# Kernel tuning notes

Measured on AMD Instinct MI355X. Metric: run time of the kernel, lower is better.

Reference implementation:

```python
import jax, jax.numpy as jnp
import numpy as np

B, S, HID, NH = 64, 197, 768, 12
DH = HID // NH  # 64
EPS = 1e-24


def setup_inputs() -> dict:
    key = jax.random.key(0)
    ks = jax.random.split(key, 20)
    def lin(i):
        w = jax.random.normal(ks[i], (HID, HID), jnp.float32) * 0.02  # stored [in, out]
        b = jnp.zeros((HID,), jnp.float32)
        return w, b
    Wmq, bmq = lin(0); Wcq, bcq = lin(1)
    Wmk, bmk = lin(2); Wck, bck = lin(3)
    Wmv, bmv = lin(4); Wcv, bcv = lin(5)
    Wmd, bmd = lin(6); Wcd, bcd = lin(7)
    return dict(
        input_mean_tensor=jax.random.normal(ks[8], (B, S, HID), jnp.float32),
        input_cov_tensor=jax.random.normal(ks[9], (B, S, HID), jnp.float32),
        Wmq=Wmq, bmq=bmq, Wcq=Wcq, bcq=bcq,
        Wmk=Wmk, bmk=bmk, Wck=Wck, bck=bck,
        Wmv=Wmv, bmv=bmv, Wcv=Wcv, bcv=bcv,
        Wmd=Wmd, bmd=bmd, Wcd=Wcd, bcd=bcd,
    )


def _heads(x):
    # [B, S, HID] -> [B, NH, S, DH]
    return x.reshape(x.shape[0], x.shape[1], NH, DH).transpose(0, 2, 1, 3)


def _merge(x):
    # [B, NH, S, DH] -> [B, S, HID]
    return x.transpose(0, 2, 1, 3).reshape(x.shape[0], x.shape[2], HID)


def wasserstein_distance_matmul(m1, c1, m2, c2):
    # all [B, NH, S, DH]; returns [B, NH, S, S]
    m1_2 = jnp.sum(m1 * m1, -1, keepdims=True)            # [B,NH,S,1]
    m2_2 = jnp.sum(m2 * m2, -1, keepdims=True)
    ret = m1_2 + jnp.swapaxes(m2_2, -1, -2) - 2.0 * jnp.einsum('bhqd,bhkd->bhqk', m1, m2)
    c1_2 = jnp.sum(c1, -1, keepdims=True)
    c2_2 = jnp.sum(c2, -1, keepdims=True)
    s1 = jnp.sqrt(jnp.clip(c1, EPS, None))
    s2 = jnp.sqrt(jnp.clip(c2, EPS, None))
    cov_ret = c1_2 + jnp.swapaxes(c2_2, -1, -2) - 2.0 * jnp.einsum('bhqd,bhkd->bhqk', s1, s2)
    return ret + cov_ret


def reference(input_mean_tensor, input_cov_tensor,
              Wmq, bmq, Wcq, bcq, Wmk, bmk, Wck, bck,
              Wmv, bmv, Wcv, bcv, Wmd, bmd, Wcd, bcd):
    mean_q = _heads(input_mean_tensor @ Wmq + bmq)
    mean_k = _heads(input_mean_tensor @ Wmk + bmk)
    mean_v = _heads(input_mean_tensor @ Wmv + bmv)
    cov_q = _heads(jax.nn.elu(input_cov_tensor @ Wcq + bcq) + 1.0)
    cov_k = _heads(jax.nn.elu(input_cov_tensor @ Wck + bck) + 1.0)
    cov_v = _heads(jax.nn.elu(input_cov_tensor @ Wcv + bcv) + 1.0)

    scores = -wasserstein_distance_matmul(mean_q, cov_q, mean_k, cov_k)
    scores = scores / jnp.sqrt(jnp.float32(DH))
    probs = jax.nn.softmax(scores, axis=-1)  # [B,NH,S,S]

    mean_ctx = _merge(jnp.einsum('bhqk,bhkd->bhqd', probs, mean_v))
    cov_ctx = _merge(jnp.einsum('bhqk,bhkd->bhqd', probs * probs, cov_v))

    mean_hidden = mean_ctx @ Wmd + bmd
    cov_hidden = cov_ctx @ Wcd + bcd
    return (mean_hidden, cov_hidden)
```

## Files before the change

### kernel.cpp

```cpp
#include <hip/hip_runtime.h>
#include <hip/hip_bf16.h>
#include <stdint.h>

typedef _Float16 f16;
typedef _Float16 f16x8 __attribute__((ext_vector_type(8)));
typedef _Float16 f16x4 __attribute__((ext_vector_type(4)));
typedef float f32x4 __attribute__((ext_vector_type(4)));

constexpr int B = 64, S = 197, HID = 768, NH = 12, DH = 64;
constexpr int M = B * S;
constexpr int Mpad = 12800;
constexpr int BNS = B * NH * S;
constexpr int VSTRIDE = 224;
constexpr size_t NPH = (size_t)Mpad * HID;
constexpr size_t MH = (size_t)M * HID;
constexpr size_t WSZ1 = (size_t)HID * HID;
constexpr size_t VTSZ = (size_t)B * NH * DH * VSTRIDE;

__device__ __forceinline__ f32x4 mfma16(f16x8 a, f16x8 b, f32x4 c) {
  return __builtin_amdgcn_mfma_f32_16x16x32_f16(a, b, c, 0, 0, 0);
}

__device__ __forceinline__ void gload16(const void* g, void* l) {
  __builtin_amdgcn_global_load_lds(
      (const __attribute__((address_space(1))) void*)g,
      (__attribute__((address_space(3))) void*)l, 16, 0, 0);
}

__device__ __forceinline__ int xcd_swizzle(int wg, int nwg) {
  const int q = nwg >> 3, r = nwg & 7;
  const int x = wg & 7, p = wg >> 3;
  return (x < r ? x * (q + 1) : r * (q + 1) + (x - r) * q) + p;
}

__global__ __launch_bounds__(256) void zero_kernel(char* __restrict__ p, size_t n16) {
  const size_t i = (size_t)blockIdx.x * 256 + threadIdx.x;
  if (i < n16) reinterpret_cast<int4*>(p)[i] = int4{0, 0, 0, 0};
}

__global__ __launch_bounds__(256) void cvt_x_kernel(
    const float* __restrict__ xm, const float* __restrict__ xc,
    f16* __restrict__ ym, f16* __restrict__ yc) {
  const size_t i8 = ((size_t)blockIdx.x * 256 + threadIdx.x) * 8;
  f16x8 vm = {}, vc = {};
  if (i8 < MH) {
    const float4 a0 = *reinterpret_cast<const float4*>(xm + i8);
    const float4 a1 = *reinterpret_cast<const float4*>(xm + i8 + 4);
    const float4 b0 = *reinterpret_cast<const float4*>(xc + i8);
    const float4 b1 = *reinterpret_cast<const float4*>(xc + i8 + 4);
    vm[0] = (f16)a0.x; vm[1] = (f16)a0.y; vm[2] = (f16)a0.z; vm[3] = (f16)a0.w;
    vm[4] = (f16)a1.x; vm[5] = (f16)a1.y; vm[6] = (f16)a1.z; vm[7] = (f16)a1.w;
    vc[0] = (f16)b0.x; vc[1] = (f16)b0.y; vc[2] = (f16)b0.z; vc[3] = (f16)b0.w;
    vc[4] = (f16)b1.x; vc[5] = (f16)b1.y; vc[6] = (f16)b1.z; vc[7] = (f16)b1.w;
  }
  *reinterpret_cast<f16x8*>(ym + i8) = vm;
  *reinterpret_cast<f16x8*>(yc + i8) = vc;
}

struct WPtrs { const float* w[8]; };

__global__ __launch_bounds__(256) void cvt_w_kernel(WPtrs p, f16* __restrict__ wt) {
  __shared__ float tile[32][33];
  const int z = blockIdx.z;
  const float* W = p.w[z];
  f16* Wt = wt + (size_t)z * WSZ1;
  const int k0 = blockIdx.x * 32, n0 = blockIdx.y * 32;
  const int tx = threadIdx.x & 31, ty = threadIdx.x >> 5;
#pragma unroll
  for (int i = 0; i < 4; ++i)
    tile[ty + i * 8][tx] = W[(size_t)(k0 + ty + i * 8) * HID + n0 + tx];
  __syncthreads();
#pragma unroll
  for (int i = 0; i < 4; ++i)
    Wt[(size_t)(n0 + ty + i * 8) * HID + k0 + tx] = (f16)tile[tx][ty + i * 8];
}

__device__ __forceinline__ void gemm_core(
    const f16* __restrict__ Abase, const f16* __restrict__ Btbase,
    int m0, int n0, int tid, char* lds, f32x4 (&acc)[4][4]) {
  const int w = tid >> 6, lane = tid & 63;
  const int l15 = lane & 15, lg = lane >> 4;
  const int wr = (w >> 2) * 64, wc = (w & 3) * 64;

  const int arow = w * 16 + (lane >> 2);
  const int brow = w * 32 + (lane >> 2);
  const int scol = (((lane & 3) ^ ((lane >> 3) & 3)) * 16);
  const char* gA = reinterpret_cast<const char*>(Abase + (size_t)(m0 + arow) * HID) + scol;
  const char* gB = reinterpret_cast<const char*>(Btbase + (size_t)(n0 + brow) * HID) + scol;

  const int rslot = ((lg ^ (l15 >> 1)) & 3) * 16;

#define STAGE_TILE(T, BUF)                                               \
  do {                                                                   \
    const size_t off_ = (size_t)(T) * 64;                                \
    char* bp_ = lds + (BUF) * 24576;                                     \
    gload16(gA + off_, bp_ + w * 1024);                                  \
    gload16(gB + off_, bp_ + 8192 + w * 2048);                           \
    gload16(gB + off_ + (size_t)16 * 1536, bp_ + 8192 + w * 2048 + 1024);\
  } while (0)

  STAGE_TILE(0, 0);
  STAGE_TILE(1, 1);
  asm volatile("s_waitcnt vmcnt(3)\n\ts_barrier" ::: "memory");

#pragma unroll
  for (int t = 0; t < 24; ++t) {
    if (t + 2 < 24) STAGE_TILE(t + 2, (t + 2) % 3);

    const char* cb = lds + (t % 3) * 24576;
    f16x8 af[4], bf[4];
#pragma unroll
    for (int fi = 0; fi < 4; ++fi)
      af[fi] = *reinterpret_cast<const f16x8*>(cb + (wr + l15 + fi * 16) * 64 + rslot);
#pragma unroll
    for (int fj = 0; fj < 4; ++fj)
      bf[fj] = *reinterpret_cast<const f16x8*>(
          cb + 8192 + (wc + l15 + fj * 16) * 64 + rslot);

    __builtin_amdgcn_s_setprio(1);
#pragma unroll
    for (int fi = 0; fi < 4; ++fi)
#pragma unroll
      for (int fj = 0; fj < 4; ++fj)
        acc[fi][fj] = mfma16(af[fi], bf[fj], acc[fi][fj]);
    __builtin_amdgcn_s_setprio(0);

    if (t + 2 < 24) {
      asm volatile("s_waitcnt vmcnt(3)\n\ts_barrier" ::: "memory");
    } else if (t + 1 < 24) {
      asm volatile("s_waitcnt vmcnt(0)\n\ts_barrier" ::: "memory");
    }
  }
#undef STAGE_TILE
}

struct ProjArgs {
  const f16* A[2]; const f16* Bt[2];
  const float* bias[2][3];
  f16* out0[2];
  f16* out1[2];
  f16* vt[2];
  float* qterm; float* kterm;
};

template <int Z>
__global__ __launch_bounds__(512, 2) void gemm_proj(ProjArgs g) {
  __shared__ alignas(16) char lds[73728];
  const int swz = xcd_swizzle(blockIdx.x, 900);
  const int x = swz / 9, y = swz - x * 9;
  const int m0 = x * 128, n0 = y * 256;

  f32x4 acc[4][4] = {};
  gemm_core(g.A[Z], g.Bt[Z], m0, n0, threadIdx.x, lds, acc);

  const int tid = threadIdx.x, w = tid >> 6, lane = tid & 63;
  const int l15 = lane & 15, lg = lane >> 4;
  const int wr = (w >> 2) * 64, wc = (w & 3) * 64;
  const int nsel = n0 / 768;
  const int colbase = (n0 - nsel * 768) + wc;
  const int rbase = m0 + wr + lg * 4;
  const float* bias = g.bias[Z][nsel];

  if (nsel < 2) {
    const int hh = colbase >> 6;
    f16* Y = nsel ? g.out1[Z] : g.out0[Z];
    float* term = nsel ? g.kterm : g.qterm;
    float bv4[4];
#pragma unroll
    for (int fj = 0; fj < 4; ++fj) bv4[fj] = bias[colbase + l15 + fj * 16];
#pragma unroll
    for (int fi = 0; fi < 4; ++fi) {
#pragma unroll
      for (int r = 0; r < 4; ++r) {
        const int row = rbase + fi * 16 + r;
        float ssum = 0.f;
#pragma unroll
        for (int fj = 0; fj < 4; ++fj) {
          float v = acc[fi][fj][r] + bv4[fj];
          if (Z == 1) { v = (v > 0.f) ? v + 1.f : __expf(v); v = sqrtf(v); }
          const f16 st = (f16)(v * 0.5f);
          if (row < M) Y[(size_t)row * HID + colbase + l15 + fj * 16] = st;
          const float sf = (float)st;
          ssum = fmaf(sf, sf, ssum);
        }
        ssum += __shfl_xor(ssum, 1, 64);
        ssum += __shfl_xor(ssum, 2, 64);
        ssum += __shfl_xor(ssum, 4, 64);
        ssum += __shfl_xor(ssum, 8, 64);
        if (l15 == 0 && row < M) {
          const int bb = row / S, ss = row - bb * S;
          atomicAdd(&term[(bb * NH + hh) * S + ss], 0.5f * ssum);
        }
      }
    }
  } else {
    f16* VT = g.vt[Z];
    f16* LT = reinterpret_cast<f16*>(lds);
    __syncthreads();
#pragma unroll
    for (int fj = 0; fj < 4; ++fj) {
      const int c = wc + l15 + fj * 16;
      const float bv = bias[colbase - wc + c];
#pragma unroll
      for (int fi = 0; fi < 4; ++fi)
#pragma unroll
        for (int r = 0; r < 4; ++r) {
          const int rl = wr - (wr & 64) + 0;
          (void)rl;
          float v = acc[fi][fj][r] + bv;
          if (Z == 1) v = (v > 0.f) ? v + 1.f : __expf(v);
          const int row_local = wr + lg * 4 + fi * 16 + r;
          LT[(size_t)c * 136 + row_local] = (f16)v;
        }
    }
    __syncthreads();
    const int rh = w >> 2;
    const int cw = w & 3;
    const int row_local = rh * 64 + lane;
    const int grow = m0 + row_local;
    if (grow < M) {
      const int bb = grow / S;
      const int ss = grow - bb * S;
      const int vb = n0 - 1536;
#pragma unroll 8
      for (int k = 0; k < 64; ++k) {
        const int c = cw * 64 + k;
        const int vcol = vb + c;
        const int hh = vcol >> 6, dd = vcol & 63;
        const f16 v = LT[(size_t)c * 136 + row_local];
        VT[((size_t)(bb * NH + hh) * DH + dd) * VSTRIDE + ss] = v;
      }
    }
  }
}

struct OutArgs {
  const f16* A[2]; const f16* Bt[2]; const float* bias[2]; float* Y[2];
};

template <int Z>
__global__ __launch_bounds__(512, 2) void gemm_out(OutArgs g) {
  __shared__ alignas(16) char lds[73728];
  const int swz = xcd_swizzle(blockIdx.x, 300);
  const int x = swz / 3, y = swz - x * 3;
  const int m0 = x * 128, n0 = y * 256;

  f32x4 acc[4][4] = {};
  gemm_core(g.A[Z], g.Bt[Z], m0, n0, threadIdx.x, lds, acc);

  const int tid = threadIdx.x, w = tid >> 6, lane = tid & 63;
  const int l15 = lane & 15, lg = lane >> 4;
  const int wr = (w >> 2) * 64, wc = (w & 3) * 64;
  const int rbase = m0 + wr + lg * 4;
  float* Y = g.Y[Z];
#pragma unroll
  for (int fj = 0; fj < 4; ++fj) {
    const int col = n0 + wc + l15 + fj * 16;
    const float bv = g.bias[Z][col];
#pragma unroll
    for (int fi = 0; fi < 4; ++fi)
#pragma unroll
      for (int r = 0; r < 4; ++r) {
        const int row = rbase + fi * 16 + r;
        if (row < M) Y[(size_t)row * HID + col] = acc[fi][fj][r] + bv;
      }
  }
}

__global__ __launch_bounds__(256, 2) void attn_kernel(
    const f16* __restrict__ mq, const f16* __restrict__ sq,
    const f16* __restrict__ mk, const f16* __restrict__ sk,
    const f16* __restrict__ vtm, const f16* __restrict__ vtc,
    const float* __restrict__ qterm, const float* __restrict__ kterm,
    f16* __restrict__ mean_ctx, f16* __restrict__ cov_ctx) {
  __shared__ char Pb[64 * 512];
  __shared__ float qt_s[64];
  __shared__ float kt_s[256];
  __shared__ float red_m[4][64];
  __shared__ float red_s[4][64];

  const int swz = xcd_swizzle(blockIdx.x, 3072);
  const int qtile = swz & 3, bh = swz >> 2;
  const int h = bh % NH, b = bh / NH;
  const int s0 = qtile * 64;
  const int tid = threadIdx.x, w = tid >> 6, lane = tid & 63;
  const int l15 = lane & 15, lg = lane >> 4;

  const size_t base = (size_t)(b * S) * HID + (size_t)h * DH;
  const int tb = bh * S;

  f16x8 qmf[4][2], qsf[4][2];
#pragma unroll
  for (int fi = 0; fi < 4; ++fi) {
    const size_t o = base + (size_t)(s0 + fi * 16 + l15) * HID + lg * 8;
    qmf[fi][0] = *reinterpret_cast<const f16x8*>(mq + o);
    qmf[fi][1] = *reinterpret_cast<const f16x8*>(mq + o + 32);
    qsf[fi][0] = *reinterpret_cast<const f16x8*>(sq + o);
    qsf[fi][1] = *reinterpret_cast<const f16x8*>(sq + o + 32);
  }
  if (tid < 64) qt_s[tid] = (s0 + tid < S) ? qterm[tb + s0 + tid] : 0.f;
  kt_s[tid] = (tid < S) ? kterm[tb + tid] : 0.f;
  __syncthreads();

  f32x4 acc[4][4] = {};
  __builtin_amdgcn_s_setprio(1);
#pragma unroll
  for (int fj = 0; fj < 4; ++fj) {
    const size_t o = base + (size_t)(w * 64 + fj * 16 + l15) * HID + lg * 8;
    const f16x8 a0 = *reinterpret_cast<const f16x8*>(mk + o);
    const f16x8 a1 = *reinterpret_cast<const f16x8*>(mk + o + 32);
    const f16x8 c0 = *reinterpret_cast<const f16x8*>(sk + o);
    const f16x8 c1 = *reinterpret_cast<const f16x8*>(sk + o + 32);
#pragma unroll
    for (int fi = 0; fi < 4; ++fi) {
      acc[fj][fi] = mfma16(a0, qmf[fi][0], acc[fj][fi]);
      acc[fj][fi] = mfma16(c0, qsf[fi][0], acc[fj][fi]);
      acc[fj][fi] = mfma16(a1, qmf[fi][1], acc[fj][fi]);
      acc[fj][fi] = mfma16(c1, qsf[fi][1], acc[fj][fi]);
    }
  }
  __builtin_amdgcn_s_setprio(0);

  const int d = w * 16 + l15;
  const size_t vbase = ((size_t)bh * DH + d) * VSTRIDE + lg * 8;
  f16x8 vmr[7], vcr[7];
#pragma unroll
  for (int ks = 0; ks < 7; ++ks) {
    vmr[ks] = *reinterpret_cast<const f16x8*>(vtm + vbase + ks * 32);
    vcr[ks] = *reinterpret_cast<const f16x8*>(vtc + vbase + ks * 32);
  }

#pragma unroll
  for (int fi = 0; fi < 4; ++fi) {
    const float qv = qt_s[fi * 16 + l15];
    float mx = -1e30f;
#pragma unroll
    for (int fj = 0; fj < 4; ++fj)
#pragma unroll
      for (int r = 0; r < 4; ++r) {
        const int j = w * 64 + fj * 16 + lg * 4 + r;
        float sv = acc[fj][fi][r] - qv - kt_s[j];
        if (j >= S) sv = -1e30f;
        acc[fj][fi][r] = sv;
        mx = fmaxf(mx, sv);
      }
    mx = fmaxf(mx, __shfl_xor(mx, 16, 64));
    mx = fmaxf(mx, __shfl_xor(mx, 32, 64));
    if (lg == 0) red_m[w][fi * 16 + l15] = mx;
  }
  __syncthreads();

#pragma unroll
  for (int fi = 0; fi < 4; ++fi) {
    const int q = fi * 16 + l15;
    const float m = fmaxf(fmaxf(red_m[0][q], red_m[1][q]),
                          fmaxf(red_m[2][q], red_m[3][q]));
    const int xr = (q & 7) << 4;
    float sum = 0.f;
#pragma unroll
    for (int fj = 0; fj < 4; ++fj) {
      f16x4 p4;
#pragma unroll
      for (int r = 0; r < 4; ++r) {
        const float e = __expf(acc[fj][fi][r] - m);
        sum += e;
        p4[r] = (f16)e;
      }
      *reinterpret_cast<f16x4*>(
          Pb + q * 512 + ((2 * (w * 64 + fj * 16 + lg * 4)) ^ xr)) = p4;
    }
    sum += __shfl_xor(sum, 16, 64);
    sum += __shfl_xor(sum, 32, 64);
    if (lg == 0) red_s[w][q] = sum;
  }
  __syncthreads();

  f32x4 macc[4] = {}, cacc[4] = {};
  __builtin_amdgcn_s_setprio(1);
#pragma unroll
  for (int ks = 0; ks < 7; ++ks) {
#pragma unroll
    for (int fi = 0; fi < 4; ++fi) {
      const int q = fi * 16 + l15;
      const f16x8 pa = *reinterpret_cast<const f16x8*>(
          Pb + q * 512 + ((2 * (ks * 32 + lg * 8)) ^ ((q & 7) << 4)));
      macc[fi] = mfma16(pa, vmr[ks], macc[fi]);
      const f16x8 pq = pa * pa;
      cacc[fi] = mfma16(pq, vcr[ks], cacc[fi]);
    }
  }
  __builtin_amdgcn_s_setprio(0);

#pragma unroll
  for (int fi = 0; fi < 4; ++fi)
#pragma unroll
    for (int r = 0; r < 4; ++r) {
      const int qo = fi * 16 + lg * 4 + r;
      const int srow = s0 + qo;
      if (srow < S) {
        const float tot = red_s[0][qo] + red_s[1][qo] + red_s[2][qo] + red_s[3][qo];
        const float inv = 1.f / tot;
        const size_t oidx = (size_t)(b * S + srow) * HID + h * DH + d;
        mean_ctx[oidx] = (f16)(macc[fi][r] * inv);
        cov_ctx[oidx] = (f16)(cacc[fi][r] * inv * inv);
      }
    }
}

extern "C" void kernel_launch(void* const* d_in, const int* in_sizes, int n_in,
                              void* d_out, int out_size, void* d_ws, size_t ws_size,
                              hipStream_t stream) {
  const float* in_mean = (const float*)d_in[0];
  const float* in_cov = (const float*)d_in[1];
  const float* Wmq = (const float*)d_in[2];  const float* bmq = (const float*)d_in[3];
  const float* Wcq = (const float*)d_in[4];  const float* bcq = (const float*)d_in[5];
  const float* Wmk = (const float*)d_in[6];  const float* bmk = (const float*)d_in[7];
  const float* Wck = (const float*)d_in[8];  const float* bck = (const float*)d_in[9];
  const float* Wmv = (const float*)d_in[10]; const float* bmv = (const float*)d_in[11];
  const float* Wcv = (const float*)d_in[12]; const float* bcv = (const float*)d_in[13];
  const float* Wmd = (const float*)d_in[14]; const float* bmd = (const float*)d_in[15];
  const float* Wcd = (const float*)d_in[16]; const float* bcd = (const float*)d_in[17];

  const size_t need = (2 * NPH + 8 * WSZ1 + 4 * MH + 2 * VTSZ) * sizeof(f16) +
                      2 * (size_t)BNS * sizeof(float);
  if (ws_size < need) return;

  f16* Xm = (f16*)d_ws;
  f16* Xc = Xm + NPH;
  f16* Wt = Xc + NPH;
  f16* mq = Wt + 8 * WSZ1;
  f16* mk = mq + MH;
  f16* sq = mk + MH;
  f16* sk = sq + MH;
  f16* vtm = sk + MH;
  f16* vtc = vtm + VTSZ;
  float* qterm = (float*)(vtc + VTSZ);
  float* kterm = qterm + BNS;
  f16* mean_ctx = Xm;
  f16* cov_ctx = Xc;

  float* out_mean = (float*)d_out;
  float* out_cov = out_mean + MH;

  dim3 blk(256);

  const size_t zbytes = 2 * VTSZ * sizeof(f16) + 2 * (size_t)BNS * sizeof(float);
  const size_t n16 = zbytes / 16;
  zero_kernel<<<(int)((n16 + 255) / 256), blk, 0, stream>>>((char*)vtm, n16);

  cvt_x_kernel<<<(int)(NPH / 2048), blk, 0, stream>>>(in_mean, in_cov, Xm, Xc);

  WPtrs wp;
  wp.w[0] = Wmq; wp.w[1] = Wmk; wp.w[2] = Wmv;
  wp.w[3] = Wcq; wp.w[4] = Wck; wp.w[5] = Wcv;
  wp.w[6] = Wmd; wp.w[7] = Wcd;
  cvt_w_kernel<<<dim3(24, 24, 8), blk, 0, stream>>>(wp, Wt);

  ProjArgs pa;
  pa.A[0] = Xm; pa.A[1] = Xc;
  pa.Bt[0] = Wt; pa.Bt[1] = Wt + 3 * WSZ1;
  pa.bias[0][0] = bmq; pa.bias[0][1] = bmk; pa.bias[0][2] = bmv;
  pa.bias[1][0] = bcq; pa.bias[1][1] = bck; pa.bias[1][2] = bcv;
  pa.out0[0] = mq; pa.out0[1] = sq;
  pa.out1[0] = mk; pa.out1[1] = sk;
  pa.vt[0] = vtm; pa.vt[1] = vtc;
  pa.qterm = qterm; pa.kterm = kterm;
  gemm_proj<0><<<900, dim3(512), 0, stream>>>(pa);
  gemm_proj<1><<<900, dim3(512), 0, stream>>>(pa);

  attn_kernel<<<3072, blk, 0, stream>>>(mq, sq, mk, sk, vtm, vtc,
                                        qterm, kterm, mean_ctx, cov_ctx);

  OutArgs oa;
  oa.A[0] = mean_ctx; oa.A[1] = cov_ctx;
  oa.Bt[0] = Wt + 6 * WSZ1; oa.Bt[1] = Wt + 7 * WSZ1;
  oa.bias[0] = bmd; oa.bias[1] = bcd;
  oa.Y[0] = out_mean; oa.Y[1] = out_cov;
  gemm_out<0><<<300, dim3(512), 0, stream>>>(oa);
  gemm_out<1><<<300, dim3(512), 0, stream>>>(oa);
}
```

Before: 366.2 us.

## Merge prep kernels, fold softmax scale into exp2, and stream V loads

Merges the zero, input-conversion and weight-transpose kernels into one prep launch that branches on block index, which removes two launch gaps. Q/K are now scaled by sqrt(log2(e)/sqrt(DH)), so the attention softmax can use exp2f directly, replacing the old 0.5 scale plus __expf. The V^T tiles are no longer all loaded into registers up front; a two-step-ahead prefetch inside the PV loop streams them, which lowers register pressure and overlaps the loads with the MFMAs. The merged prep kernel mixes different block workloads in a single grid.

```diff
diff --git a/kernel.cpp b/kernel.cpp
--- a/kernel.cpp
+++ b/kernel.cpp
@@ -17,6 +17,8 @@
 constexpr size_t WSZ1 = (size_t)HID * HID;
 constexpr size_t VTSZ = (size_t)B * NH * DH * VSTRIDE;
 
+#define QK_SCALE 0.6005612f
+
 __device__ __forceinline__ f32x4 mfma16(f16x8 a, f16x8 b, f32x4 c) {
   return __builtin_amdgcn_mfma_f32_16x16x32_f16(a, b, c, 0, 0, 0);
 }
@@ -33,46 +35,53 @@
   return (x < r ? x * (q + 1) : r * (q + 1) + (x - r) * q) + p;
 }
 
-__global__ __launch_bounds__(256) void zero_kernel(char* __restrict__ p, size_t n16) {
-  const size_t i = (size_t)blockIdx.x * 256 + threadIdx.x;
-  if (i < n16) reinterpret_cast<int4*>(p)[i] = int4{0, 0, 0, 0};
-}
-
-__global__ __launch_bounds__(256) void cvt_x_kernel(
-    const float* __restrict__ xm, const float* __restrict__ xc,
-    f16* __restrict__ ym, f16* __restrict__ yc) {
-  const size_t i8 = ((size_t)blockIdx.x * 256 + threadIdx.x) * 8;
-  f16x8 vm = {}, vc = {};
-  if (i8 < MH) {
-    const float4 a0 = *reinterpret_cast<const float4*>(xm + i8);
-    const float4 a1 = *reinterpret_cast<const float4*>(xm + i8 + 4);
-    const float4 b0 = *reinterpret_cast<const float4*>(xc + i8);
-    const float4 b1 = *reinterpret_cast<const float4*>(xc + i8 + 4);
-    vm[0] = (f16)a0.x; vm[1] = (f16)a0.y; vm[2] = (f16)a0.z; vm[3] = (f16)a0.w;
-    vm[4] = (f16)a1.x; vm[5] = (f16)a1.y; vm[6] = (f16)a1.z; vm[7] = (f16)a1.w;
-    vc[0] = (f16)b0.x; vc[1] = (f16)b0.y; vc[2] = (f16)b0.z; vc[3] = (f16)b0.w;
-    vc[4] = (f16)b1.x; vc[5] = (f16)b1.y; vc[6] = (f16)b1.z; vc[7] = (f16)b1.w;
-  }
-  *reinterpret_cast<f16x8*>(ym + i8) = vm;
-  *reinterpret_cast<f16x8*>(yc + i8) = vc;
-}
-
 struct WPtrs { const float* w[8]; };
-
-__global__ __launch_bounds__(256) void cvt_w_kernel(WPtrs p, f16* __restrict__ wt) {
+struct PrepArgs {
+  char* zp; size_t zn16;
+  const float* xm; const float* xc; f16* ym; f16* yc;
+  WPtrs wp; f16* wt;
+};
+
+__global__ __launch_bounds__(256) void prep_kernel(PrepArgs p) {
   __shared__ float tile[32][33];
-  const int z = blockIdx.z;
-  const float* W = p.w[z];
-  f16* Wt = wt + (size_t)z * WSZ1;
-  const int k0 = blockIdx.x * 32, n0 = blockIdx.y * 32;
-  const int tx = threadIdx.x & 31, ty = threadIdx.x >> 5;
-#pragma unroll
-  for (int i = 0; i < 4; ++i)
-    tile[ty + i * 8][tx] = W[(size_t)(k0 + ty + i * 8) * HID + n0 + tx];
-  __syncthreads();
-#pragma unroll
-  for (int i = 0; i < 4; ++i)
-    Wt[(size_t)(n0 + ty + i * 8) * HID + k0 + tx] = (f16)tile[tx][ty + i * 8];
+  const int nz = (int)((p.zn16 + 255) / 256);
+  const int nc = (int)(NPH / 2048);
+  const int bid = blockIdx.x;
+  if (bid < nz) {
+    const size_t i = (size_t)bid * 256 + threadIdx.x;
+    if (i < p.zn16) reinterpret_cast<int4*>(p.zp)[i] = int4{0, 0, 0, 0};
+  } else if (bid < nz + nc) {
+    const size_t i8 = ((size_t)(bid - nz) * 256 + threadIdx.x) * 8;
+    f16x8 vm = {}, vc = {};
+    if (i8 < MH) {
+      const float4 a0 = *reinterpret_cast<const float4*>(p.xm + i8);
+      const float4 a1 = *reinterpret_cast<const float4*>(p.xm + i8 + 4);
+      const float4 b0 = *reinterpret_cast<const float4*>(p.xc + i8);
+      const float4 b1 = *reinterpret_cast<const float4*>(p.xc + i8 + 4);
+      vm[0] = (f16)a0.x; vm[1] = (f16)a0.y; vm[2] = (f16)a0.z; vm[3] = (f16)a0.w;
+      vm[4] = (f16)a1.x; vm[5] = (f16)a1.y; vm[6] = (f16)a1.z; vm[7] = (f16)a1.w;
+      vc[0] = (f16)b0.x; vc[1] = (f16)b0.y; vc[2] = (f16)b0.z; vc[3] = (f16)b0.w;
+      vc[4] = (f16)b1.x; vc[5] = (f16)b1.y; vc[6] = (f16)b1.z; vc[7] = (f16)b1.w;
+    }
+    *reinterpret_cast<f16x8*>(p.ym + i8) = vm;
+    *reinterpret_cast<f16x8*>(p.yc + i8) = vc;
+  } else {
+    const int t = bid - nz - nc;
+    const int z = t / 576;
+    const int rest = t - z * 576;
+    const int kx = rest / 24, ny = rest - kx * 24;
+    const float* W = p.wp.w[z];
+    f16* Wt = p.wt + (size_t)z * WSZ1;
+    const int k0 = kx * 32, n0 = ny * 32;
+    const int tx = threadIdx.x & 31, ty = threadIdx.x >> 5;
+#pragma unroll
+    for (int i = 0; i < 4; ++i)
+      tile[ty + i * 8][tx] = W[(size_t)(k0 + ty + i * 8) * HID + n0 + tx];
+    __syncthreads();
+#pragma unroll
+    for (int i = 0; i < 4; ++i)
+      Wt[(size_t)(n0 + ty + i * 8) * HID + k0 + tx] = (f16)tile[tx][ty + i * 8];
+  }
 }
 
 __device__ __forceinline__ void gemm_core(
@@ -178,7 +187,7 @@
         for (int fj = 0; fj < 4; ++fj) {
           float v = acc[fi][fj][r] + bv4[fj];
           if (Z == 1) { v = (v > 0.f) ? v + 1.f : __expf(v); v = sqrtf(v); }
-          const f16 st = (f16)(v * 0.5f);
+          const f16 st = (f16)(v * QK_SCALE);
           if (row < M) Y[(size_t)row * HID + colbase + l15 + fj * 16] = st;
           const float sf = (float)st;
           ssum = fmaf(sf, sf, ssum);
@@ -205,8 +214,6 @@
       for (int fi = 0; fi < 4; ++fi)
 #pragma unroll
         for (int r = 0; r < 4; ++r) {
-          const int rl = wr - (wr & 64) + 0;
-          (void)rl;
           float v = acc[fi][fj][r] + bv;
           if (Z == 1) v = (v > 0.f) ? v + 1.f : __expf(v);
           const int row_local = wr + lg * 4 + fi * 16 + r;
@@ -321,15 +328,6 @@
   }
   __builtin_amdgcn_s_setprio(0);
 
-  const int d = w * 16 + l15;
-  const size_t vbase = ((size_t)bh * DH + d) * VSTRIDE + lg * 8;
-  f16x8 vmr[7], vcr[7];
-#pragma unroll
-  for (int ks = 0; ks < 7; ++ks) {
-    vmr[ks] = *reinterpret_cast<const f16x8*>(vtm + vbase + ks * 32);
-    vcr[ks] = *reinterpret_cast<const f16x8*>(vtc + vbase + ks * 32);
-  }
-
 #pragma unroll
   for (int fi = 0; fi < 4; ++fi) {
     const float qv = qt_s[fi * 16 + l15];
@@ -350,6 +348,13 @@
   }
   __syncthreads();
 
+  const int d = w * 16 + l15;
+  const size_t vbase = ((size_t)bh * DH + d) * VSTRIDE + lg * 8;
+  f16x8 vm0 = *reinterpret_cast<const f16x8*>(vtm + vbase);
+  f16x8 vc0 = *reinterpret_cast<const f16x8*>(vtc + vbase);
+  f16x8 vm1 = *reinterpret_cast<const f16x8*>(vtm + vbase + 32);
+  f16x8 vc1 = *reinterpret_cast<const f16x8*>(vtc + vbase + 32);
+
 #pragma unroll
   for (int fi = 0; fi < 4; ++fi) {
     const int q = fi * 16 + l15;
@@ -362,7 +367,7 @@
       f16x4 p4;
 #pragma unroll
       for (int r = 0; r < 4; ++r) {
-        const float e = __expf(acc[fj][fi][r] - m);
+        const float e = exp2f(acc[fj][fi][r] - m);
         sum += e;
         p4[r] = (f16)e;
       }
@@ -376,20 +381,27 @@
   __syncthreads();
 
   f32x4 macc[4] = {}, cacc[4] = {};
-  __builtin_amdgcn_s_setprio(1);
+  f16x8 vmN, vcN;
 #pragma unroll
   for (int ks = 0; ks < 7; ++ks) {
+    if (ks + 2 < 7) {
+      vmN = *reinterpret_cast<const f16x8*>(vtm + vbase + (ks + 2) * 32);
+      vcN = *reinterpret_cast<const f16x8*>(vtc + vbase + (ks + 2) * 32);
+    }
+    __builtin_amdgcn_s_setprio(1);
 #pragma unroll
     for (int fi = 0; fi < 4; ++fi) {
       const int q = fi * 16 + l15;
       const f16x8 pa = *reinterpret_cast<const f16x8*>(
           Pb + q * 512 + ((2 * (ks * 32 + lg * 8)) ^ ((q & 7) << 4)));
-      macc[fi] = mfma16(pa, vmr[ks], macc[fi]);
+      macc[fi] = mfma16(pa, vm0, macc[fi]);
       const f16x8 pq = pa * pa;
-      cacc[fi] = mfma16(pq, vcr[ks], cacc[fi]);
-    }
-  }
-  __builtin_amdgcn_s_setprio(0);
+      cacc[fi] = mfma16(pq, vc0, cacc[fi]);
+    }
+    __builtin_amdgcn_s_setprio(0);
+    vm0 = vm1; vc0 = vc1;
+    vm1 = vmN; vc1 = vcN;
+  }
 
 #pragma unroll
   for (int fi = 0; fi < 4; ++fi)
@@ -444,17 +456,17 @@
 
   dim3 blk(256);
 
-  const size_t zbytes = 2 * VTSZ * sizeof(f16) + 2 * (size_t)BNS * sizeof(float);
-  const size_t n16 = zbytes / 16;
-  zero_kernel<<<(int)((n16 + 255) / 256), blk, 0, stream>>>((char*)vtm, n16);
-
-  cvt_x_kernel<<<(int)(NPH / 2048), blk, 0, stream>>>(in_mean, in_cov, Xm, Xc);
-
-  WPtrs wp;
-  wp.w[0] = Wmq; wp.w[1] = Wmk; wp.w[2] = Wmv;
-  wp.w[3] = Wcq; wp.w[4] = Wck; wp.w[5] = Wcv;
-  wp.w[6] = Wmd; wp.w[7] = Wcd;
-  cvt_w_kernel<<<dim3(24, 24, 8), blk, 0, stream>>>(wp, Wt);
+  PrepArgs pp;
+  pp.zp = (char*)vtm;
+  pp.zn16 = (2 * VTSZ * sizeof(f16) + 2 * (size_t)BNS * sizeof(float)) / 16;
+  pp.xm = in_mean; pp.xc = in_cov; pp.ym = Xm; pp.yc = Xc;
+  pp.wp.w[0] = Wmq; pp.wp.w[1] = Wmk; pp.wp.w[2] = Wmv;
+  pp.wp.w[3] = Wcq; pp.wp.w[4] = Wck; pp.wp.w[5] = Wcv;
+  pp.wp.w[6] = Wmd; pp.wp.w[7] = Wcd;
+  pp.wt = Wt;
+  const int nz = (int)((pp.zn16 + 255) / 256);
+  const int nc = (int)(NPH / 2048);
+  prep_kernel<<<nz + nc + 4608, blk, 0, stream>>>(pp);
 
   ProjArgs pa;
   pa.A[0] = Xm; pa.A[1] = Xc;
```

New measurement: 351.7 us. -3.9%, faster.
